# Kernel optimization log

Hardware: AMD Instinct MI355X
Metric: run time of the kernel (lower is better)

The kernel has to match this reference:

```python
import jax, jax.numpy as jnp
import numpy as np

B, L, C, H = 32, 641, 768, 12
MEM = 128  # memory slots K; state token at index K; tokens are causal after that


def _block_mask(L, K):
    # rows i attend to cols j per FusedAttention:
    #  memory rows (i<K): attend to memory+state (j<=K)
    #  state row (i==K): attends to everything
    #  token rows (i>K): attend to memory+state (j<=K) and causally to tokens (K<j<=i)
    i = jnp.arange(L)[:, None]
    j = jnp.arange(L)[None, :]
    mem_rows = (i < K) & (j <= K)
    state_row = (i == K)
    tok_rows = (i > K) & ((j <= K) | ((j > K) & (j <= i)))
    return mem_rows | state_row | tok_rows  # (L, L) bool


def setup_inputs() -> dict:
    key = jax.random.key(0)
    k1, k2, k3 = jax.random.split(key, 3)
    x = jax.random.normal(k1, (B, L, C), dtype=jnp.float32)
    W_attn = jax.random.normal(k2, (C, 3 * C), dtype=jnp.float32) * 0.02
    W_proj = jax.random.normal(k3, (C, C), dtype=jnp.float32) * 0.02
    return {"x": x, "W_attn": W_attn, "W_proj": W_proj, "mem_size": MEM}


def reference(x, W_attn, W_proj, mem_size):
    Bb, Ll, Cc = x.shape
    hd = Cc // H
    qkv = x @ W_attn  # (B, L, 3C)
    q, k, v = jnp.split(qkv, 3, axis=-1)
    # (B, H, L, hd)
    q = q.reshape(Bb, Ll, H, hd).transpose(0, 2, 1, 3)
    k = k.reshape(Bb, Ll, H, hd).transpose(0, 2, 1, 3)
    v = v.reshape(Bb, Ll, H, hd).transpose(0, 2, 1, 3)
    mask = _block_mask(Ll, mem_size)  # (L, L)
    scale = 1.0 / jnp.sqrt(jnp.asarray(hd, dtype=x.dtype))
    att = jnp.einsum("bhqd,bhkd->bhqk", q, k) * scale
    att = jnp.where(mask[None, None, :, :], att, jnp.asarray(-jnp.inf, att.dtype))
    att = jax.nn.softmax(att, axis=-1)
    y = jnp.einsum("bhqk,bhkd->bhqd", att, v)
    y = y.transpose(0, 2, 1, 3).reshape(Bb, Ll, Cc)
    return y @ W_proj
```

## Files before the change

### kernel.cpp

```cpp
#include <hip/hip_runtime.h>
#include <stdint.h>

#define B_SZ 32
#define L_SZ 641
#define C_SZ 768
#define H_SZ 12
#define HD 64
#define MEMK 128
#define M_REAL (B_SZ * L_SZ)
#define M_PAD 20608
#define N_QKV (3 * C_SZ)
#define NQT 11
#define QK_STRIDE 1536
#define VT_STRIDE 648
#define SCL_LOG2E 0.18033688f
#define FIXED_MAX 8.0f

typedef __attribute__((ext_vector_type(8))) short short8;
typedef __attribute__((ext_vector_type(4))) float f32x4;
typedef __attribute__((ext_vector_type(4))) unsigned short ushort4v;

__device__ inline unsigned short f2bf(float x) {
  union { float f; uint32_t u; } v; v.f = x;
  uint32_t r = v.u + 0x7fffu + ((v.u >> 16) & 1u);
  return (unsigned short)(r >> 16);
}
__device__ inline float bf2f(short v) {
  union { float f; uint32_t u; } x; x.u = ((uint32_t)(unsigned short)v) << 16;
  return x.f;
}

__device__ inline void gload_lds16(const void* g, void* l) {
  __builtin_amdgcn_global_load_lds(
      (const __attribute__((address_space(1))) uint32_t*)g,
      (__attribute__((address_space(3))) uint32_t*)l, 16, 0, 0);
}

__global__ __launch_bounds__(256) void k_conv_x(const float* __restrict__ src,
                                                unsigned short* __restrict__ dst,
                                                int n4) {
  int i = blockIdx.x * 256 + threadIdx.x;
  if (i >= n4) return;
  float4 v = *(const float4*)(src + (size_t)i * 4);
  ushort4v o = { f2bf(v.x), f2bf(v.y), f2bf(v.z), f2bf(v.w) };
  *(ushort4v*)(dst + (size_t)i * 4) = o;
}

__global__ __launch_bounds__(256) void k_transpose_bf16(const float* __restrict__ src,
                                                        unsigned short* __restrict__ dst,
                                                        int R, int Ccol,
                                                        float scale, int scale_cmax) {
  __shared__ float tile[32][33];
  int c0 = blockIdx.x * 32, r0 = blockIdx.y * 32;
  int tx = threadIdx.x & 31, ty = threadIdx.x >> 5;
  for (int i = ty; i < 32; i += 8)
    tile[i][tx] = src[(size_t)(r0 + i) * Ccol + c0 + tx];
  __syncthreads();
  float sc = (c0 < scale_cmax) ? scale : 1.0f;
  for (int i = ty; i < 32; i += 8)
    dst[(size_t)(c0 + i) * R + r0 + tx] = f2bf(tile[tx][i] * sc);
}

template <int MODE>
__global__ __launch_bounds__(256) void k_gemm(const short* __restrict__ A,
                                              const short* __restrict__ Bt,
                                              void* __restrict__ Cp,
                                              short* __restrict__ vt,
                                              int Mreal, int N, int K) {
  __shared__ short As[2][128 * 64];
  __shared__ short Bs[2][128 * 64];
  int nwg = gridDim.x;
  int qq = nwg >> 3, rr = nwg & 7;
  int x8 = blockIdx.x & 7, i8 = blockIdx.x >> 3;
  int wg = (x8 < rr ? x8 * (qq + 1) : rr * (qq + 1) + (x8 - rr) * qq) + i8;
  const int tiles_n = N >> 7;
  int tm = wg / tiles_n, tn = wg % tiles_n;
  int m0 = tm << 7, n0 = tn << 7;
  int lane = threadIdx.x & 63, wave = threadIdx.x >> 6;
  int wr = wave >> 1, wc = wave & 1;
  int l15 = lane & 15, g = lane >> 4;

  f32x4 acc[4][4];
  f32x4 z = {0.f, 0.f, 0.f, 0.f};
#pragma unroll
  for (int i = 0; i < 4; ++i)
#pragma unroll
    for (int j = 0; j < 4; ++j) acc[i][j] = z;

  int arow = lane >> 3;
  int acol = (lane & 7) * 8;

#define STAGE(K0, BUF)                                                        \
  {                                                                           \
    _Pragma("unroll")                                                         \
    for (int cc = 0; cc < 4; ++cc) {                                          \
      int rb = (cc * 4 + wave) * 8;                                           \
      gload_lds16(A + (size_t)(m0 + rb + arow) * K + ((K0) + acol),           \
                  (char*)As[BUF] + rb * 128);                                 \
      gload_lds16(Bt + (size_t)(n0 + rb + arow) * K + ((K0) + acol),          \
                  (char*)Bs[BUF] + rb * 128);                                 \
    }                                                                         \
  }

  STAGE(0, 0);
  int nk = K >> 6;
  for (int t = 0; t < nk; ++t) {
    int buf = t & 1;
    __syncthreads();
    if (t + 1 < nk) STAGE((t + 1) << 6, buf ^ 1);
#pragma unroll
    for (int ks = 0; ks < 2; ++ks) {
      short8 a[4], b[4];
      if (MODE == 3) {
#pragma unroll
        for (int nf = 0; nf < 4; ++nf)
          a[nf] = *(const short8*)&Bs[buf][(wr * 64 + nf * 16 + l15) * 64 + ks * 32 + g * 8];
#pragma unroll
        for (int mf = 0; mf < 4; ++mf)
          b[mf] = *(const short8*)&As[buf][(wc * 64 + mf * 16 + l15) * 64 + ks * 32 + g * 8];
      } else {
#pragma unroll
        for (int mf = 0; mf < 4; ++mf)
          a[mf] = *(const short8*)&As[buf][(wr * 64 + mf * 16 + l15) * 64 + ks * 32 + g * 8];
#pragma unroll
        for (int nf = 0; nf < 4; ++nf)
          b[nf] = *(const short8*)&Bs[buf][(wc * 64 + nf * 16 + l15) * 64 + ks * 32 + g * 8];
      }
#pragma unroll
      for (int i = 0; i < 4; ++i)
#pragma unroll
        for (int j = 0; j < 4; ++j)
          acc[i][j] = __builtin_amdgcn_mfma_f32_16x16x32_bf16(a[i], b[j], acc[i][j], 0, 0, 0);
    }
  }
#undef STAGE

  if (MODE == 3) {
#pragma unroll
    for (int nf = 0; nf < 4; ++nf) {
#pragma unroll
      for (int reg = 0; reg < 4; ++reg) {
        int n = n0 + wr * 64 + nf * 16 + g * 4 + reg;
        int h = n >> 6, d = n & 63;
#pragma unroll
        for (int mf = 0; mf < 4; ++mf) {
          int m = m0 + wc * 64 + mf * 16 + l15;
          if (m >= Mreal) continue;
          int bb = (unsigned)m / 641u;
          int key = m - bb * 641;
          vt[((size_t)(bb * H_SZ + h) * HD + d) * VT_STRIDE + key] = f2bf(acc[nf][mf][reg]);
        }
      }
    }
    return;
  }
#pragma unroll
  for (int mf = 0; mf < 4; ++mf) {
#pragma unroll
    for (int reg = 0; reg < 4; ++reg) {
      int m = m0 + wr * 64 + mf * 16 + g * 4 + reg;
      if (m >= Mreal) continue;
#pragma unroll
      for (int nf = 0; nf < 4; ++nf) {
        int n = n0 + wc * 64 + nf * 16 + l15;
        float v = acc[mf][nf][reg];
        if (MODE == 2)
          ((unsigned short*)Cp)[(size_t)m * QK_STRIDE + n] = f2bf(v);
        else
          ((float*)Cp)[(size_t)m * N + n] = v;
      }
    }
  }
}

__global__ __launch_bounds__(256) void k_attn(const short* __restrict__ qk,
                                              const short* __restrict__ vt,
                                              short* __restrict__ y) {
  __shared__ short Ks[2][64 * 64];
  __shared__ short Vt[2][64 * 64];
  __shared__ short Ps[4][16 * 64];

  int bid = blockIdx.x;
  int work = (bid & 7) * 528 + (bid >> 3);
  int qt = work % NQT;
  int rem = work / NQT;
  int h = rem % H_SZ;
  int b = rem / H_SZ;
  int q0 = qt * 64;
  int lane = threadIdx.x & 63, w = threadIdx.x >> 6;
  int l15 = lane & 15, g = lane >> 4;

  size_t qbase = (size_t)(b * L_SZ + q0 + w * 16 + l15) * QK_STRIDE + h * HD;
  short8 qa[2];
#pragma unroll
  for (int ks = 0; ks < 2; ++ks)
    qa[ks] = *(const short8*)&qk[qbase + ks * 32 + g * 8];

  f32x4 o[4];
  float l_run[4];
  f32x4 z = {0.f, 0.f, 0.f, 0.f};
  f32x4 m8 = {-FIXED_MAX, -FIXED_MAX, -FIXED_MAX, -FIXED_MAX};
#pragma unroll
  for (int df = 0; df < 4; ++df) o[df] = z;
#pragma unroll
  for (int r = 0; r < 4; ++r) l_run[r] = 0.f;

  int jmax[4];
#pragma unroll
  for (int reg = 0; reg < 4; ++reg) {
    int i = q0 + w * 16 + g * 4 + reg;
    jmax[reg] = (i == MEMK) ? (L_SZ - 1) : (i < MEMK ? MEMK : i);
  }
  int imin = q0 + w * 16;
  int jm_min = (imin <= MEMK) ? MEMK : imin;

  int q1 = q0 + 63; if (q1 > L_SZ - 1) q1 = L_SZ - 1;
  int col_max = (q0 <= MEMK && MEMK <= q1) ? (L_SZ - 1) : (q1 < MEMK ? MEMK : q1);

  size_t kbase = (size_t)b * L_SZ * QK_STRIDE + C_SZ + h * HD;
  size_t vbase = (size_t)(b * H_SZ + h) * HD * VT_STRIDE;

  short8 kreg[2], vreg[2];
  int i0 = threadIdx.x >> 3, j0e = (threadIdx.x & 7) * 8;
  int i1 = (threadIdx.x + 256) >> 3, j1e = j0e;
  int woff0 = i0 * 128 + ((j0e * 2) ^ ((i0 & 7) << 4));
  int woff1 = i1 * 128 + ((j1e * 2) ^ ((i1 & 7) << 4));
  int rswz = (l15 & 7) << 4;

  kreg[0] = *(const short8*)&qk[kbase + (size_t)i0 * QK_STRIDE + j0e];
  kreg[1] = *(const short8*)&qk[kbase + (size_t)i1 * QK_STRIDE + j1e];
  vreg[0] = *(const short8*)&vt[vbase + (size_t)i0 * VT_STRIDE + j0e];
  vreg[1] = *(const short8*)&vt[vbase + (size_t)i1 * VT_STRIDE + j1e];

  int nt = col_max >> 6;
  for (int t = 0; t <= nt; ++t) {
    int c0 = t << 6;
    int buf = t & 1;
    *(short8*)((char*)Ks[buf] + woff0) = kreg[0];
    *(short8*)((char*)Ks[buf] + woff1) = kreg[1];
    *(short8*)((char*)Vt[buf] + woff0) = vreg[0];
    *(short8*)((char*)Vt[buf] + woff1) = vreg[1];
    __syncthreads();
    if (t < nt) {
      int c1 = c0 + 64;
      kreg[0] = *(const short8*)&qk[kbase + (size_t)(c1 + i0) * QK_STRIDE + j0e];
      kreg[1] = *(const short8*)&qk[kbase + (size_t)(c1 + i1) * QK_STRIDE + j1e];
      vreg[0] = *(const short8*)&vt[vbase + (size_t)i0 * VT_STRIDE + c1 + j0e];
      vreg[1] = *(const short8*)&vt[vbase + (size_t)i1 * VT_STRIDE + c1 + j1e];
    }

    f32x4 s[4];
#pragma unroll
    for (int kf = 0; kf < 4; ++kf) {
      f32x4 sa = m8;
#pragma unroll
      for (int ks = 0; ks < 2; ++ks) {
        short8 kb = *(const short8*)((char*)Ks[buf] +
                        (kf * 16 + l15) * 128 + ((ks * 64 + g * 16) ^ rswz));
        sa = __builtin_amdgcn_mfma_f32_16x16x32_bf16(qa[ks], kb, sa, 0, 0, 0);
      }
      s[kf] = sa;
    }

    if (c0 + 63 > jm_min) {
#pragma unroll
      for (int kf = 0; kf < 4; ++kf) {
        int j = c0 + kf * 16 + l15;
#pragma unroll
        for (int reg = 0; reg < 4; ++reg)
          s[kf][reg] = (j <= jmax[reg]) ? s[kf][reg] : -1e30f;
      }
    }

#pragma unroll
    for (int kf = 0; kf < 4; ++kf)
#pragma unroll
      for (int reg = 0; reg < 4; ++reg)
        s[kf][reg] = exp2f(s[kf][reg]);
#pragma unroll
    for (int reg = 0; reg < 4; ++reg)
      l_run[reg] += (s[0][reg] + s[1][reg]) + (s[2][reg] + s[3][reg]);

#pragma unroll
    for (int reg = 0; reg < 4; ++reg) {
      int q = g * 4 + reg;
      char* prow = (char*)Ps[w] + q * 128;
      int qswz = (q & 7) << 4;
#pragma unroll
      for (int kf = 0; kf < 4; kf += 2) {
        uint32_t r;
        asm("v_cvt_pk_bf16_f32 %0, %1, %2"
            : "=v"(r) : "v"(s[kf][reg]), "v"(s[kf + 1][reg]));
        *(short*)(prow + ((kf * 32 + l15 * 2) ^ qswz)) = (short)(r & 0xffff);
        *(short*)(prow + (((kf + 1) * 32 + l15 * 2) ^ qswz)) = (short)(r >> 16);
      }
    }

    short8 pa[2];
#pragma unroll
    for (int ks = 0; ks < 2; ++ks)
      pa[ks] = *(const short8*)((char*)Ps[w] + l15 * 128 + ((ks * 64 + g * 16) ^ rswz));
#pragma unroll
    for (int df = 0; df < 4; ++df) {
#pragma unroll
      for (int ks = 0; ks < 2; ++ks) {
        short8 vb = *(const short8*)((char*)Vt[buf] +
                        (df * 16 + l15) * 128 + ((ks * 64 + g * 16) ^ rswz));
        o[df] = __builtin_amdgcn_mfma_f32_16x16x32_bf16(pa[ks], vb, o[df], 0, 0, 0);
      }
    }
  }

#pragma unroll
  for (int reg = 0; reg < 4; ++reg) {
    float ls = l_run[reg];
    ls += __shfl_xor(ls, 1);
    ls += __shfl_xor(ls, 2);
    ls += __shfl_xor(ls, 4);
    ls += __shfl_xor(ls, 8);
    int i = q0 + w * 16 + g * 4 + reg;
    if (i >= L_SZ) continue;
    float inv = 1.0f / ls;
#pragma unroll
    for (int df = 0; df < 4; ++df)
      y[(size_t)(b * L_SZ + i) * C_SZ + h * HD + df * 16 + l15] = (short)f2bf(o[df][reg] * inv);
  }
}

extern "C" void kernel_launch(void* const* d_in, const int* in_sizes, int n_in,
                              void* d_out, int out_size, void* d_ws, size_t ws_size,
                              hipStream_t stream) {
  const float* x = (const float*)d_in[0];
  const float* Wa = (const float*)d_in[1];
  const float* Wp = (const float*)d_in[2];
  float* out = (float*)d_out;

  char* ws = (char*)d_ws;
  size_t off0 = 0;
  short* x_bf = (short*)(ws + off0);
  size_t off1 = off0 + (size_t)M_PAD * C_SZ * 2;
  short* Wa_t = (short*)(ws + off1);
  size_t off2 = off1 + (size_t)N_QKV * C_SZ * 2;
  short* Wp_t = (short*)(ws + off2);
  size_t off3 = off2 + (size_t)C_SZ * C_SZ * 2;
  short* qk = (short*)(ws + off3);
  size_t off4 = off3 + (size_t)M_REAL * QK_STRIDE * 2;
  short* vt = (short*)(ws + off4);
  size_t need = off4 + (size_t)B_SZ * H_SZ * HD * VT_STRIDE * 2 + 4096;
  if (ws_size < need) return;

  int n4 = M_REAL * C_SZ / 4;
  k_conv_x<<<(n4 + 255) / 256, 256, 0, stream>>>(x, (unsigned short*)x_bf, n4);
  k_transpose_bf16<<<dim3(N_QKV / 32, C_SZ / 32), 256, 0, stream>>>(
      Wa, (unsigned short*)Wa_t, C_SZ, N_QKV, SCL_LOG2E, C_SZ);
  k_transpose_bf16<<<dim3(C_SZ / 32, C_SZ / 32), 256, 0, stream>>>(
      Wp, (unsigned short*)Wp_t, C_SZ, C_SZ, 1.0f, 0);

  k_gemm<2><<<(M_PAD / 128) * (QK_STRIDE / 128), 256, 0, stream>>>(
      x_bf, Wa_t, (void*)qk, nullptr, M_REAL, QK_STRIDE, C_SZ);
  k_gemm<3><<<(M_PAD / 128) * (C_SZ / 128), 256, 0, stream>>>(
      x_bf, Wa_t + (size_t)QK_STRIDE * C_SZ, nullptr, vt, M_REAL, C_SZ, C_SZ);
  k_attn<<<B_SZ * H_SZ * NQT, 256, 0, stream>>>(qk, vt, x_bf );
  k_gemm<0><<<(M_PAD / 128) * (C_SZ / 128), 256, 0, stream>>>(
      x_bf, Wp_t, (void*)out, nullptr, M_REAL, C_SZ, C_SZ);
}
```

Before: 271.7 us.

## Pre-swizzle K/V in GEMM epilogue and stage attention tiles via direct global-to-LDS loads

The QKV GEMM epilogue now writes K and V^T with an XOR swizzle already applied to the column index, so the attention kernel can copy tiles straight into LDS with direct global-to-LDS loads (gload_lds16) instead of going through registers. This drops the register staging and the separate swizzled ds_write, and lets the loads for the next tile overlap compute. The last partial V tile (keys at 640 and above) is left unswizzled, which needs special cases in both kernels. The change depends on the swizzle conventions matching exactly across the two kernels.

Measured after the change: 278.6 us. 1.03x slower.

```diff
diff --git a/kernel.cpp b/kernel.cpp
--- a/kernel.cpp
+++ b/kernel.cpp
@@ -142,13 +142,15 @@
       for (int reg = 0; reg < 4; ++reg) {
         int n = n0 + wr * 64 + nf * 16 + g * 4 + reg;
         int h = n >> 6, d = n & 63;
+        int xr = (d & 7) << 3;
 #pragma unroll
         for (int mf = 0; mf < 4; ++mf) {
           int m = m0 + wc * 64 + mf * 16 + l15;
           if (m >= Mreal) continue;
           int bb = (unsigned)m / 641u;
           int key = m - bb * 641;
-          vt[((size_t)(bb * H_SZ + h) * HD + d) * VT_STRIDE + key] = f2bf(acc[nf][mf][reg]);
+          int k2 = (key >= 640) ? key : (key ^ xr);
+          vt[((size_t)(bb * H_SZ + h) * HD + d) * VT_STRIDE + k2] = f2bf(acc[nf][mf][reg]);
         }
       }
     }
@@ -160,13 +162,20 @@
     for (int reg = 0; reg < 4; ++reg) {
       int m = m0 + wr * 64 + mf * 16 + g * 4 + reg;
       if (m >= Mreal) continue;
+      int xr = 0;
+      if (MODE == 2) {
+        int bb = (unsigned)m / 641u;
+        int key = m - bb * 641;
+        xr = (key & 7) << 3;
+      }
 #pragma unroll
       for (int nf = 0; nf < 4; ++nf) {
         int n = n0 + wc * 64 + nf * 16 + l15;
         float v = acc[mf][nf][reg];
-        if (MODE == 2)
-          ((unsigned short*)Cp)[(size_t)m * QK_STRIDE + n] = f2bf(v);
-        else
+        if (MODE == 2) {
+          int nn = (n >= C_SZ) ? (n ^ xr) : n;
+          ((unsigned short*)Cp)[(size_t)m * QK_STRIDE + nn] = f2bf(v);
+        } else
           ((float*)Cp)[(size_t)m * N + n] = v;
       }
     }
@@ -220,34 +229,31 @@
   size_t kbase = (size_t)b * L_SZ * QK_STRIDE + C_SZ + h * HD;
   size_t vbase = (size_t)(b * H_SZ + h) * HD * VT_STRIDE;
 
-  short8 kreg[2], vreg[2];
   int i0 = threadIdx.x >> 3, j0e = (threadIdx.x & 7) * 8;
   int i1 = (threadIdx.x + 256) >> 3, j1e = j0e;
-  int woff0 = i0 * 128 + ((j0e * 2) ^ ((i0 & 7) << 4));
-  int woff1 = i1 * 128 + ((j1e * 2) ^ ((i1 & 7) << 4));
   int rswz = (l15 & 7) << 4;
 
-  kreg[0] = *(const short8*)&qk[kbase + (size_t)i0 * QK_STRIDE + j0e];
-  kreg[1] = *(const short8*)&qk[kbase + (size_t)i1 * QK_STRIDE + j1e];
-  vreg[0] = *(const short8*)&vt[vbase + (size_t)i0 * VT_STRIDE + j0e];
-  vreg[1] = *(const short8*)&vt[vbase + (size_t)i1 * VT_STRIDE + j1e];
+#define STAGE_ATTN(C0, BUF)                                                   \
+  {                                                                           \
+    gload_lds16(qk + kbase + (size_t)((C0) + i0) * QK_STRIDE + j0e,           \
+                (char*)Ks[BUF] + w * 1024);                                   \
+    gload_lds16(qk + kbase + (size_t)((C0) + i1) * QK_STRIDE + j1e,           \
+                (char*)Ks[BUF] + w * 1024 + 4096);                            \
+    gload_lds16(vt + vbase + (size_t)i0 * VT_STRIDE + (C0) + j0e,             \
+                (char*)Vt[BUF] + w * 1024);                                   \
+    gload_lds16(vt + vbase + (size_t)i1 * VT_STRIDE + (C0) + j1e,             \
+                (char*)Vt[BUF] + w * 1024 + 4096);                            \
+  }
+
+  STAGE_ATTN(0, 0);
 
   int nt = col_max >> 6;
   for (int t = 0; t <= nt; ++t) {
     int c0 = t << 6;
     int buf = t & 1;
-    *(short8*)((char*)Ks[buf] + woff0) = kreg[0];
-    *(short8*)((char*)Ks[buf] + woff1) = kreg[1];
-    *(short8*)((char*)Vt[buf] + woff0) = vreg[0];
-    *(short8*)((char*)Vt[buf] + woff1) = vreg[1];
     __syncthreads();
-    if (t < nt) {
-      int c1 = c0 + 64;
-      kreg[0] = *(const short8*)&qk[kbase + (size_t)(c1 + i0) * QK_STRIDE + j0e];
-      kreg[1] = *(const short8*)&qk[kbase + (size_t)(c1 + i1) * QK_STRIDE + j1e];
-      vreg[0] = *(const short8*)&vt[vbase + (size_t)i0 * VT_STRIDE + c1 + j0e];
-      vreg[1] = *(const short8*)&vt[vbase + (size_t)i1 * VT_STRIDE + c1 + j1e];
-    }
+    if (t < nt) STAGE_ATTN(c0 + 64, buf ^ 1);
+    int vswz = (c0 >= 640) ? 0 : rswz;
 
     f32x4 s[4];
 #pragma unroll
@@ -305,11 +311,12 @@
 #pragma unroll
       for (int ks = 0; ks < 2; ++ks) {
         short8 vb = *(const short8*)((char*)Vt[buf] +
-                        (df * 16 + l15) * 128 + ((ks * 64 + g * 16) ^ rswz));
+                        (df * 16 + l15) * 128 + ((ks * 64 + g * 16) ^ vswz));
         o[df] = __builtin_amdgcn_mfma_f32_16x16x32_bf16(pa[ks], vb, o[df], 0, 0, 0);
       }
     }
   }
+#undef STAGE_ATTN
 
 #pragma unroll
   for (int reg = 0; reg < 4; ++reg) {
```
